# Performance work log

Measured on AMD Instinct MI355X. Metric: run time of the kernel, lower is better.

## Reference

```python
import jax, jax.numpy as jnp
import numpy as np

EPS = 1e-5  # BatchNorm2d default eps


def _binarize_ste(x):
    """Forward: sign(x). Backward: hardtanh STE (grad 1 where |x|<=1, else 0)."""
    xc = jnp.clip(x, -1.0, 1.0)
    return xc + jax.lax.stop_gradient(jnp.sign(x) - xc)


def setup_inputs() -> dict:
    key = jax.random.key(0)
    k1, k2, k3, k4 = jax.random.split(key, 4)
    x = jax.random.normal(k1, (32, 256, 32, 32), dtype=jnp.float32)
    # BatchNorm affine params (affine=True)
    gamma = 1.0 + 0.1 * jax.random.normal(k2, (256,), dtype=jnp.float32)
    beta = 0.1 * jax.random.normal(k3, (256,), dtype=jnp.float32)
    # Conv weight, OIHW, bias=False
    W = 0.05 * jax.random.normal(k4, (256, 256, 3, 3), dtype=jnp.float32)
    return {"x": x, "gamma": gamma, "beta": beta, "W": W}


def reference(x, gamma, beta, W):
    # BatchNorm2d, training-mode batch statistics over (N, H, W) per channel
    mean = jnp.mean(x, axis=(0, 2, 3), keepdims=True)
    var = jnp.var(x, axis=(0, 2, 3), keepdims=True)
    xn = (x - mean) * jax.lax.rsqrt(var + EPS)
    xn = xn * gamma[None, :, None, None] + beta[None, :, None, None]
    # Conv2d_1w1a: binarize activations and weights (sign fwd / STE bwd), then conv
    a = _binarize_ste(xn)
    wb = _binarize_ste(W)
    out = jax.lax.conv_general_dilated(
        a, wb,
        window_strides=(1, 1),
        padding=((1, 1), (1, 1)),
        dimension_numbers=("NCHW", "OIHW", "NCHW"),
    )
    return out
```

## Files before the change

### kernel.cpp

```cpp
#include <hip/hip_runtime.h>
#include <hip/hip_bf16.h>


#define NIMG 32
#define C    256
#define K    256

typedef int v4i  __attribute__((ext_vector_type(4)));
typedef int v16i __attribute__((ext_vector_type(16)));

#define AHT_IMG 295936
#define AHT_KB  36992
#define AHT_ROW 1088


__global__ __launch_bounds__(256) void k_stats_packw(
    const float* __restrict__ x, const float* __restrict__ W,
    double2* __restrict__ partials, char* __restrict__ wfrag) {
  int bx = blockIdx.x;
  int tid = threadIdx.x;
  if (bx >= 2048) {
    int k = bx - 2048, c = tid;
    const float* src = W + ((size_t)k * 256 + c) * 9;
    char* dst = wfrag + (size_t)(c >> 4) * 4096 + k * 16 + (c & 15);
    #pragma unroll
    for (int t = 0; t < 9; ++t)
      dst[(size_t)t * 65536] = (src[t] > 0.0f) ? (char)1 : (char)-1;
    return;
  }
  int c = bx >> 3, grp = bx & 7;
  double s = 0.0, sq = 0.0;
  #pragma unroll
  for (int ni = 0; ni < 4; ++ni) {
    int n = grp * 4 + ni;
    const float* p = x + (size_t)n * (C * 1024) + (size_t)c * 1024;
    float4 v = ((const float4*)p)[tid];
    s += (double)v.x + (double)v.y + (double)v.z + (double)v.w;
    sq += (double)v.x * v.x + (double)v.y * v.y
        + (double)v.z * v.z + (double)v.w * v.w;
  }
  for (int o = 32; o > 0; o >>= 1) {
    s += __shfl_down(s, o);
    sq += __shfl_down(sq, o);
  }
  __shared__ double ls[4], lq[4];
  if ((tid & 63) == 0) { ls[tid >> 6] = s; lq[tid >> 6] = sq; }
  __syncthreads();
  if (tid == 0) {
    double2 r;
    r.x = ls[0] + ls[1] + ls[2] + ls[3];
    r.y = lq[0] + lq[1] + lq[2] + lq[3];
    partials[c * 8 + grp] = r;
  }
}

__global__ __launch_bounds__(256) void k_packa_i8(
    const float* __restrict__ x, const double2* __restrict__ partials,
    const float* __restrict__ gamma, const float* __restrict__ beta,
    char* __restrict__ aHT) {
  __shared__ float lf[32 * 257];
  __shared__ float lthr[256];
  __shared__ unsigned lfl[256];
  int y = blockIdx.x, n = blockIdx.y, tid = threadIdx.x;

  {
    double S = 0.0, Q = 0.0;
    #pragma unroll
    for (int g = 0; g < 8; ++g) {
      double2 p = partials[tid * 8 + g];
      S += p.x; Q += p.y;
    }
    const double N = 32768.0;
    double mean = S / N;
    double var = Q / N - mean * mean;
    double rs = 1.0 / sqrt(var + 1e-5);
    double gm = (double)gamma[tid];
    double bt = (double)beta[tid];
    float t;
    unsigned flip;
    if (gm == 0.0) {
      t = (bt > 0.0) ? -3.0e38f : 3.0e38f;
      flip = 0u;
    } else {
      t = (float)(mean - bt / (rs * gm));
      flip = (gm < 0.0) ? 1u : 0u;
    }
    lthr[tid] = t;
    lfl[tid] = flip;
  }

  #pragma unroll
  for (int it = 0; it < 8; ++it) {
    int c = it * 32 + (tid >> 3), q = tid & 7;
    float4 v = *(const float4*)(x + (size_t)n * 262144 + (size_t)c * 1024
                                + y * 32 + q * 4);
    lf[(q * 4 + 0) * 257 + c] = v.x;
    lf[(q * 4 + 1) * 257 + c] = v.y;
    lf[(q * 4 + 2) * 257 + c] = v.z;
    lf[(q * 4 + 3) * 257 + c] = v.w;
  }
  __syncthreads();
  int xl = tid & 31, cb = tid >> 5;
  unsigned wds[8];
  #pragma unroll
  for (int g = 0; g < 8; ++g) {
    unsigned wv = 0;
    #pragma unroll
    for (int jj = 0; jj < 4; ++jj) {
      int c = cb * 32 + g * 4 + jj;
      float v = lf[xl * 257 + c];
      unsigned bit = ((v > lthr[c]) ? 1u : 0u) ^ lfl[c];
      unsigned byte = bit ? 0x01u : 0xFFu;
      wv |= byte << (8 * jj);
    }
    wds[g] = wv;
  }
  char* dst = aHT + ((size_t)n * 8 + cb) * AHT_KB
            + (size_t)(y + 1) * AHT_ROW + (size_t)(xl + 1) * 32;
  uint4 u0, u1;
  u0.x = wds[0]; u0.y = wds[1]; u0.z = wds[2]; u0.w = wds[3];
  u1.x = wds[4]; u1.y = wds[5]; u1.z = wds[6]; u1.w = wds[7];
  *(uint4*)dst = u0;
  *((uint4*)dst + 1) = u1;

  uint4 z; z.x = 0; z.y = 0; z.z = 0; z.w = 0;
  if (xl < 2) {
    char* hz = aHT + ((size_t)n * 8 + cb) * AHT_KB
             + (size_t)(y + 1) * AHT_ROW + (size_t)(xl * 33) * 32;
    *(uint4*)hz = z;
    *((uint4*)hz + 1) = z;
  }
  if (y == 0 || y == 31) {
    int row = (y == 0) ? 0 : 33;
    for (int idx = tid; idx < 272; idx += 256) {
      int kb = idx / 34, xx = idx % 34;
      char* hz = aHT + ((size_t)n * 8 + kb) * AHT_KB
               + (size_t)row * AHT_ROW + (size_t)xx * 32;
      *(uint4*)hz = z;
      *((uint4*)hz + 1) = z;
    }
  }
}

__global__ __launch_bounds__(512) void k_conv_mfma(
    const char* __restrict__ aHT, const char* __restrict__ wfrag,
    float* __restrict__ out) {
  int tid = threadIdx.x;
  int lane = tid & 63, w = tid >> 6;
  int nh = w & 3, mb = w >> 2;
  int bx = blockIdx.x;
  int lb = (bx & 7) * 32 + (bx >> 3);
  int n = lb >> 3, ys = lb & 7;
  int yw = ys * 4 + mb * 2;
  int xl = lane & 31, hi = lane >> 5;

  const char* abT = aHT + (size_t)n * AHT_IMG + (size_t)(xl + 1) * 32 + hi * 16;
  const char* wB = wfrag + hi * 4096 + (nh * 64 + xl) * 16;

  v16i a00 = {0}, a01 = {0}, a10 = {0}, a11 = {0};
  v4i cA00, cA01, cA10, cA11, nA00, nA01, nA10, nA11;
  v4i cB0, cB1, cB2, cB3, nB0, nB1, nB2, nB3;

  {
    const char* ab = abT + (size_t)yw * AHT_ROW - 32;
    cA00 = *(const v4i*)(ab);
    cA01 = *(const v4i*)(ab + AHT_ROW);
    cA10 = *(const v4i*)(ab + AHT_KB);
    cA11 = *(const v4i*)(ab + AHT_KB + AHT_ROW);
    cB0 = *(const v4i*)(wB);
    cB1 = *(const v4i*)(wB + 512);
    cB2 = *(const v4i*)(wB + 8192);
    cB3 = *(const v4i*)(wB + 8192 + 512);
  }

  for (int p = 0; p < 36; ++p) {
    if (p < 35) {
      int pp = p + 1;
      int tt = pp >> 2;
      int kb0 = (pp & 3) * 2;
      int dy = tt / 3 - 1, dx = tt % 3 - 1;
      const char* ab = abT + (size_t)kb0 * AHT_KB
                     + (size_t)(yw + dy + 1) * AHT_ROW + dx * 32;
      nA00 = *(const v4i*)(ab);
      nA01 = *(const v4i*)(ab + AHT_ROW);
      nA10 = *(const v4i*)(ab + AHT_KB);
      nA11 = *(const v4i*)(ab + AHT_KB + AHT_ROW);
      const char* wp2 = wB + (size_t)pp * 16384;
      nB0 = *(const v4i*)(wp2);
      nB1 = *(const v4i*)(wp2 + 512);
      nB2 = *(const v4i*)(wp2 + 8192);
      nB3 = *(const v4i*)(wp2 + 8192 + 512);
    }
    a00 = __builtin_amdgcn_mfma_i32_32x32x32_i8(cA00, cB0, a00, 0, 0, 0);
    a01 = __builtin_amdgcn_mfma_i32_32x32x32_i8(cA00, cB1, a01, 0, 0, 0);
    a10 = __builtin_amdgcn_mfma_i32_32x32x32_i8(cA01, cB0, a10, 0, 0, 0);
    a11 = __builtin_amdgcn_mfma_i32_32x32x32_i8(cA01, cB1, a11, 0, 0, 0);
    a00 = __builtin_amdgcn_mfma_i32_32x32x32_i8(cA10, cB2, a00, 0, 0, 0);
    a01 = __builtin_amdgcn_mfma_i32_32x32x32_i8(cA10, cB3, a01, 0, 0, 0);
    a10 = __builtin_amdgcn_mfma_i32_32x32x32_i8(cA11, cB2, a10, 0, 0, 0);
    a11 = __builtin_amdgcn_mfma_i32_32x32x32_i8(cA11, cB3, a11, 0, 0, 0);
    if (p < 35) {
      cA00 = nA00; cA01 = nA01; cA10 = nA10; cA11 = nA11;
      cB0 = nB0; cB1 = nB1; cB2 = nB2; cB3 = nB3;
    }
  }

  size_t ob0 = (size_t)n * 262144 + (size_t)(nh * 64 + xl) * 1024
             + (size_t)yw * 32 + 4 * hi;
  #pragma unroll
  for (int r = 0; r < 2; ++r) {
    #pragma unroll
    for (int nb = 0; nb < 2; ++nb) {
      v16i av = (r == 0) ? (nb == 0 ? a00 : a01) : (nb == 0 ? a10 : a11);
      float* obp = out + ob0 + (size_t)nb * 32768 + r * 32;
      #pragma unroll
      for (int q = 0; q < 4; ++q) {
        float4 f;
        f.x = (float)av[q * 4 + 0];
        f.y = (float)av[q * 4 + 1];
        f.z = (float)av[q * 4 + 2];
        f.w = (float)av[q * 4 + 3];
        *(float4*)(obp + 8 * q) = f;
      }
    }
  }
}


__global__ __launch_bounds__(256) void k_stats_part_fb(
    const float* __restrict__ x, double2* __restrict__ partials) {
  int grp = blockIdx.x;
  int c = blockIdx.y;
  int tid = threadIdx.x;
  double s = 0.0, sq = 0.0;
  #pragma unroll
  for (int ni = 0; ni < 4; ++ni) {
    int n = grp * 4 + ni;
    const float* p = x + (size_t)n * (C * 1024) + (size_t)c * 1024;
    float4 v = ((const float4*)p)[tid];
    s += (double)v.x + (double)v.y + (double)v.z + (double)v.w;
    sq += (double)v.x * v.x + (double)v.y * v.y
        + (double)v.z * v.z + (double)v.w * v.w;
  }
  for (int o = 32; o > 0; o >>= 1) {
    s += __shfl_down(s, o);
    sq += __shfl_down(sq, o);
  }
  __shared__ double ls[4], lq[4];
  if ((tid & 63) == 0) { ls[tid >> 6] = s; lq[tid >> 6] = sq; }
  __syncthreads();
  if (tid == 0) {
    double2 r;
    r.x = ls[0] + ls[1] + ls[2] + ls[3];
    r.y = lq[0] + lq[1] + lq[2] + lq[3];
    partials[c * 8 + grp] = r;
  }
}

__global__ __launch_bounds__(256) void k_packw_corr_final(
    const float* __restrict__ W, const double2* __restrict__ partials,
    const float* __restrict__ gamma, const float* __restrict__ beta,
    unsigned* __restrict__ wp, int* __restrict__ corr,
    unsigned* __restrict__ zp, float* __restrict__ t_out,
    unsigned* __restrict__ flip_out) {
  int bk = blockIdx.x;
  int tid = threadIdx.x;
  if (bk == 256) {
    int c = tid;
    double S = 0.0, Q = 0.0;
    #pragma unroll
    for (int g = 0; g < 8; ++g) {
      double2 p = partials[c * 8 + g];
      S += p.x; Q += p.y;
    }
    const double N = 32768.0;
    double mean = S / N;
    double var = Q / N - mean * mean;
    double rs = 1.0 / sqrt(var + 1e-5);
    double g = (double)gamma[c];
    double b = (double)beta[c];
    float t;
    unsigned flip;
    if (g == 0.0) {
      t = (b > 0.0) ? -3.0e38f : 3.0e38f;
      flip = 0u;
    } else {
      t = (float)(mean - b / (rs * g));
      flip = (g < 0.0) ? 1u : 0u;
    }
    t_out[c] = t;
    flip_out[c] = flip;
    return;
  }
  int k = bk;
  __shared__ unsigned lw[72];
  float w[9];
  const float* src = W + (size_t)k * 2304 + (size_t)tid * 9;
  #pragma unroll
  for (int t = 0; t < 9; ++t) w[t] = src[t];
  int lane = tid & 63, wv = tid >> 6;
  #pragma unroll
  for (int t = 0; t < 9; ++t) {
    unsigned long long m = __ballot(w[t] > 0.0f);
    if (lane == 0) {
      lw[t * 8 + 2 * wv] = (unsigned)m;
      lw[t * 8 + 2 * wv + 1] = (unsigned)(m >> 32);
    }
  }
  __syncthreads();
  if (tid < 72) wp[(size_t)k * 72 + tid] = lw[tid];
  if (tid >= 128 && tid < 144) {
    int cls = tid - 128;
    int sum = 0;
    #pragma unroll
    for (int t = 0; t < 9; ++t) {
      int dy = t / 3 - 1, dx = t % 3 - 1;
      bool inv = (((cls & 1) && dx == -1) || ((cls & 2) && dx == 1) ||
                  ((cls & 4) && dy == -1) || ((cls & 8) && dy == 1));
      if (inv) {
        #pragma unroll
        for (int j = 0; j < 8; ++j) sum += __popc(lw[t * 8 + j]);
      }
    }
    corr[k * 16 + cls] = sum;
  }
  if (bk == 0 && tid >= 192 && tid < 200) zp[tid - 192] = 0u;
}

__global__ __launch_bounds__(256) void k_packa_bits(
    const float* __restrict__ x, const float* __restrict__ t,
    const unsigned* __restrict__ flip, unsigned* __restrict__ ap) {
  int n = blockIdx.y;
  int p0 = blockIdx.x * 64;
  int pix = threadIdx.x & 63;
  int q = threadIdx.x >> 6;
  unsigned w0 = 0, w1 = 0;
  const float* xb = x + (size_t)n * (C * 1024) + p0 + pix;
  #pragma unroll
  for (int i = 0; i < 64; ++i) {
    int c = q * 64 + i;
    float tv = t[c];
    unsigned fl = flip[c];
    float v = xb[(size_t)c * 1024];
    unsigned bit = ((v > tv) ? 1u : 0u) ^ fl;
    if (i < 32) w0 |= bit << i;
    else        w1 |= bit << (i - 32);
  }
  uint2 st; st.x = w0; st.y = w1;
  *(uint2*)(ap + ((size_t)n * 1024 + p0 + pix) * 8 + q * 2) = st;
}

__global__ __launch_bounds__(256) void k_conv_pop(
    const unsigned* __restrict__ ap, const unsigned* __restrict__ wp,
    const int* __restrict__ corr, const unsigned* __restrict__ zp,
    float* __restrict__ out) {
  int n = blockIdx.z;
  int ystrip = blockIdx.y;
  int kc = blockIdx.x;
  int tid = threadIdx.x;
  int lane = tid & 63;
  int wave = tid >> 6;
  int y = ystrip * 8 + wave * 2 + (lane >> 5);
  int xx = lane & 31;
  int cls = (xx == 0 ? 1 : 0) | (xx == 31 ? 2 : 0) |
            (y == 0 ? 4 : 0) | (y == 31 ? 8 : 0);
  uint4 a0[9], a1[9];
  int nv = 0;
  const uint4* zp4 = (const uint4*)zp;
  #pragma unroll
  for (int t = 0; t < 9; ++t) {
    int dy = t / 3 - 1, dx = t % 3 - 1;
    int cy = y + dy, cx = xx + dx;
    bool valid = (cy >= 0) & (cy < 32) & (cx >= 0) & (cx < 32);
    nv += valid ? 1 : 0;
    const uint4* pa = valid
        ? (const uint4*)(ap + (((size_t)n * 32 + cy) * 32 + cx) * 8)
        : zp4;
    a0[t] = pa[0];
    a1[t] = pa[1];
  }
  int bias = nv << 8;
  float* ob = out + (size_t)n * (K * 1024) + (size_t)y * 32 + xx;
  for (int kk = 0; kk < 16; ++kk) {
    int k = kc * 16 + kk;
    const uint4* wq = (const uint4*)(wp + (size_t)k * 72);
    int s0 = 0, s1 = 0, s2 = 0, s3 = 0, s4 = 0, s5 = 0, s6 = 0, s7 = 0;
    #pragma unroll
    for (int t = 0; t < 9; ++t) {
      uint4 wa = wq[t * 2];
      uint4 wb = wq[t * 2 + 1];
      s0 += __popc(a0[t].x ^ wa.x);
      s1 += __popc(a0[t].y ^ wa.y);
      s2 += __popc(a0[t].z ^ wa.z);
      s3 += __popc(a0[t].w ^ wa.w);
      s4 += __popc(a1[t].x ^ wb.x);
      s5 += __popc(a1[t].y ^ wb.y);
      s6 += __popc(a1[t].z ^ wb.z);
      s7 += __popc(a1[t].w ^ wb.w);
    }
    int S = ((s0 + s1) + (s2 + s3)) + ((s4 + s5) + (s6 + s7));
    int tot = corr[(k << 4) + cls] - S;
    ob[(size_t)k * 1024] = (float)(bias + 2 * tot);
  }
}


extern "C" void kernel_launch(void* const* d_in, const int* in_sizes, int n_in,
                              void* d_out, int out_size, void* d_ws, size_t ws_size,
                              hipStream_t stream) {
  const float* x = (const float*)d_in[0];
  const float* gamma = (const float*)d_in[1];
  const float* beta = (const float*)d_in[2];
  const float* W = (const float*)d_in[3];
  float* out = (float*)d_out;
  char* ws = (char*)d_ws;

  const size_t NEED = 655360 + (size_t)NIMG * AHT_IMG;
  if (ws_size >= NEED) {
    double2* partials = (double2*)(ws + 4096);
    char* wfrag = ws + 36864;
    char* aHT = ws + 655360;

    k_stats_packw<<<2304, 256, 0, stream>>>(x, W, partials, wfrag);
    k_packa_i8<<<dim3(32, 32), 256, 0, stream>>>(x, partials, gamma, beta, aHT);
    k_conv_mfma<<<256, 512, 0, stream>>>(aHT, wfrag, out);
  } else {
    float* t = (float*)ws;
    unsigned* flip = (unsigned*)(ws + 1024);
    unsigned* wp = (unsigned*)(ws + 4096);
    unsigned* zp = (unsigned*)(ws + 77824);
    int* corr = (int*)(ws + 78336);
    double2* partials = (double2*)(ws + 98304);
    unsigned* ap = (unsigned*)(ws + 131072);

    k_stats_part_fb<<<dim3(8, 256), 256, 0, stream>>>(x, partials);
    k_packw_corr_final<<<257, 256, 0, stream>>>(W, partials, gamma, beta,
                                                wp, corr, zp, t, flip);
    k_packa_bits<<<dim3(16, 32), 256, 0, stream>>>(x, t, flip, ap);
    k_conv_pop<<<dim3(16, 4, 32), 256, 0, stream>>>(ap, wp, corr, zp, out);
  }
}
```

Baseline: 49.87 us.

## Stage conv A/B tiles in LDS via async global_load_lds double buffering

Rewrites the conv MFMA main loop so each step's activation and weight fragments are copied from global memory straight into a double-buffered LDS tile with global_load_lds. Warps then read their operands from LDS instead of issuing redundant per-warp global loads. Operands that several warps share are fetched once per block, cutting global/L2 traffic. The cost is 48KB of shared memory per block, which may limit occupancy, plus a block-wide barrier every iteration.

```diff
diff --git a/kernel.cpp b/kernel.cpp
--- a/kernel.cpp
+++ b/kernel.cpp
@@ -12,6 +12,10 @@
 #define AHT_IMG 295936
 #define AHT_KB  36992
 #define AHT_ROW 1088
+
+#define GL16(gp, lp) __builtin_amdgcn_global_load_lds(                        \
+    (const __attribute__((address_space(1))) unsigned int*)(gp),              \
+    (__attribute__((address_space(3))) unsigned int*)(lp), 16, 0, 0)
 
 
 __global__ __launch_bounds__(256) void k_stats_packw(
@@ -145,64 +149,74 @@
 __global__ __launch_bounds__(512) void k_conv_mfma(
     const char* __restrict__ aHT, const char* __restrict__ wfrag,
     float* __restrict__ out) {
+  __shared__ char As[49152];
   int tid = threadIdx.x;
   int lane = tid & 63, w = tid >> 6;
   int nh = w & 3, mb = w >> 2;
   int bx = blockIdx.x;
   int lb = (bx & 7) * 32 + (bx >> 3);
   int n = lb >> 3, ys = lb & 7;
-  int yw = ys * 4 + mb * 2;
+  int y0 = ys * 4;
+  int yw = y0 + mb * 2;
   int xl = lane & 31, hi = lane >> 5;
 
-  const char* abT = aHT + (size_t)n * AHT_IMG + (size_t)(xl + 1) * 32 + hi * 16;
-  const char* wB = wfrag + hi * 4096 + (nh * 64 + xl) * 16;
+  int sr = w >> 1, skb = w & 1;
+  int sp = lane & 31, sh = lane >> 5;
+  const char* aLane = aHT + (size_t)n * AHT_IMG + (size_t)skb * AHT_KB
+                    + (size_t)sp * 32 + sh * 16;
+
+  unsigned aRd = (unsigned)(mb * 4096 + hi * 512 + xl * 16);
+  unsigned bRd = (unsigned)(hi * 4096 + (nh * 64 + xl) * 16);
 
   v16i a00 = {0}, a01 = {0}, a10 = {0}, a11 = {0};
-  v4i cA00, cA01, cA10, cA11, nA00, nA01, nA10, nA11;
-  v4i cB0, cB1, cB2, cB3, nB0, nB1, nB2, nB3;
 
   {
-    const char* ab = abT + (size_t)yw * AHT_ROW - 32;
-    cA00 = *(const v4i*)(ab);
-    cA01 = *(const v4i*)(ab + AHT_ROW);
-    cA10 = *(const v4i*)(ab + AHT_KB);
-    cA11 = *(const v4i*)(ab + AHT_KB + AHT_ROW);
-    cB0 = *(const v4i*)(wB);
-    cB1 = *(const v4i*)(wB + 512);
-    cB2 = *(const v4i*)(wB + 8192);
-    cB3 = *(const v4i*)(wB + 8192 + 512);
-  }
+    const char* ag = aLane + (size_t)(y0 + 0 + sr) * AHT_ROW + 0;
+    GL16(ag, As + w * 1024);
+    const char* bg = wfrag + (size_t)(2 * w) * 1024 + lane * 16;
+    GL16(bg, As + 8192 + (2 * w) * 1024);
+    GL16(bg + 1024, As + 8192 + (2 * w + 1) * 1024);
+  }
+  __syncthreads();
 
   for (int p = 0; p < 36; ++p) {
+    int cur = (p & 1) * 24576;
     if (p < 35) {
+      int nxt = 24576 - cur;
       int pp = p + 1;
       int tt = pp >> 2;
       int kb0 = (pp & 3) * 2;
       int dy = tt / 3 - 1, dx = tt % 3 - 1;
-      const char* ab = abT + (size_t)kb0 * AHT_KB
-                     + (size_t)(yw + dy + 1) * AHT_ROW + dx * 32;
-      nA00 = *(const v4i*)(ab);
-      nA01 = *(const v4i*)(ab + AHT_ROW);
-      nA10 = *(const v4i*)(ab + AHT_KB);
-      nA11 = *(const v4i*)(ab + AHT_KB + AHT_ROW);
-      const char* wp2 = wB + (size_t)pp * 16384;
-      nB0 = *(const v4i*)(wp2);
-      nB1 = *(const v4i*)(wp2 + 512);
-      nB2 = *(const v4i*)(wp2 + 8192);
-      nB3 = *(const v4i*)(wp2 + 8192 + 512);
-    }
-    a00 = __builtin_amdgcn_mfma_i32_32x32x32_i8(cA00, cB0, a00, 0, 0, 0);
-    a01 = __builtin_amdgcn_mfma_i32_32x32x32_i8(cA00, cB1, a01, 0, 0, 0);
-    a10 = __builtin_amdgcn_mfma_i32_32x32x32_i8(cA01, cB0, a10, 0, 0, 0);
-    a11 = __builtin_amdgcn_mfma_i32_32x32x32_i8(cA01, cB1, a11, 0, 0, 0);
-    a00 = __builtin_amdgcn_mfma_i32_32x32x32_i8(cA10, cB2, a00, 0, 0, 0);
-    a01 = __builtin_amdgcn_mfma_i32_32x32x32_i8(cA10, cB3, a01, 0, 0, 0);
-    a10 = __builtin_amdgcn_mfma_i32_32x32x32_i8(cA11, cB2, a10, 0, 0, 0);
-    a11 = __builtin_amdgcn_mfma_i32_32x32x32_i8(cA11, cB3, a11, 0, 0, 0);
-    if (p < 35) {
-      cA00 = nA00; cA01 = nA01; cA10 = nA10; cA11 = nA11;
-      cB0 = nB0; cB1 = nB1; cB2 = nB2; cB3 = nB3;
-    }
+      const char* ag = aLane + (size_t)kb0 * AHT_KB
+                     + (size_t)(y0 + 1 + dy + sr) * AHT_ROW
+                     + (size_t)(1 + dx) * 32;
+      GL16(ag, As + nxt + w * 1024);
+      const char* bg = wfrag + (size_t)pp * 16384 + (size_t)(2 * w) * 1024
+                     + lane * 16;
+      GL16(bg, As + nxt + 8192 + (2 * w) * 1024);
+      GL16(bg + 1024, As + nxt + 8192 + (2 * w + 1) * 1024);
+    }
+    {
+      const char* cb = As + cur;
+      v4i A00 = *(const v4i*)(cb + aRd);
+      v4i A01 = *(const v4i*)(cb + aRd + 1024);
+      v4i A10 = *(const v4i*)(cb + aRd + 2048);
+      v4i A11 = *(const v4i*)(cb + aRd + 3072);
+      const char* bb = cb + 8192;
+      v4i B0 = *(const v4i*)(bb + bRd);
+      v4i B1 = *(const v4i*)(bb + bRd + 512);
+      v4i B2 = *(const v4i*)(bb + bRd + 8192);
+      v4i B3 = *(const v4i*)(bb + bRd + 8192 + 512);
+      a00 = __builtin_amdgcn_mfma_i32_32x32x32_i8(A00, B0, a00, 0, 0, 0);
+      a01 = __builtin_amdgcn_mfma_i32_32x32x32_i8(A00, B1, a01, 0, 0, 0);
+      a10 = __builtin_amdgcn_mfma_i32_32x32x32_i8(A10, B0, a10, 0, 0, 0);
+      a11 = __builtin_amdgcn_mfma_i32_32x32x32_i8(A10, B1, a11, 0, 0, 0);
+      a00 = __builtin_amdgcn_mfma_i32_32x32x32_i8(A01, B2, a00, 0, 0, 0);
+      a01 = __builtin_amdgcn_mfma_i32_32x32x32_i8(A01, B3, a01, 0, 0, 0);
+      a10 = __builtin_amdgcn_mfma_i32_32x32x32_i8(A11, B2, a10, 0, 0, 0);
+      a11 = __builtin_amdgcn_mfma_i32_32x32x32_i8(A11, B3, a11, 0, 0, 0);
+    }
+    __syncthreads();
   }
 
   size_t ob0 = (size_t)n * 262144 + (size_t)(nh * 64 + xl) * 1024
```

Result: slower. 53.98 us (+8.2%).

## Stage activation halo tile in LDS and deepen weight prefetch

Applied to the files above, without the earlier changes.

The conv kernel now cooperatively copies the block's binarized activation tile (6 rows with halo, all 8 channel blocks, 34 columns) into about 52KB of shared memory once. It then reads the A fragments for each tap from LDS instead of issuing repeated global loads per tap. Weight fragments are now prefetched two iterations ahead instead of one. This trades roughly 9x redundant global/L2 traffic for LDS reads plus a barrier, but the large LDS footprint may reduce occupancy and the LDS access pattern may cause bank conflicts.

```diff
diff --git a/kernel.cpp b/kernel.cpp
--- a/kernel.cpp
+++ b/kernel.cpp
@@ -145,65 +145,73 @@
 __global__ __launch_bounds__(512) void k_conv_mfma(
     const char* __restrict__ aHT, const char* __restrict__ wfrag,
     float* __restrict__ out) {
+  __shared__ uint4 As4[3264];
+  char* As = (char*)As4;
   int tid = threadIdx.x;
   int lane = tid & 63, w = tid >> 6;
   int nh = w & 3, mb = w >> 2;
   int bx = blockIdx.x;
   int lb = (bx & 7) * 32 + (bx >> 3);
   int n = lb >> 3, ys = lb & 7;
-  int yw = ys * 4 + mb * 2;
+  int y0 = ys * 4;
+  int yw = y0 + mb * 2;
   int xl = lane & 31, hi = lane >> 5;
 
-  const char* abT = aHT + (size_t)n * AHT_IMG + (size_t)(xl + 1) * 32 + hi * 16;
+  {
+    const char* aImg = aHT + (size_t)n * AHT_IMG;
+    for (int e = tid; e < 3264; e += 512) {
+      int px = e % 34;
+      int q = e / 34;
+      int hs = q & 1;
+      int q2 = q >> 1;
+      int rl = q2 % 6;
+      int kb = q2 / 6;
+      const char* g = aImg + (size_t)kb * AHT_KB
+                    + (size_t)(y0 + rl) * AHT_ROW + px * 32 + hs * 16;
+      *(v4i*)(As + (size_t)e * 16) = *(const v4i*)g;
+    }
+  }
+  __syncthreads();
+
   const char* wB = wfrag + hi * 4096 + (nh * 64 + xl) * 16;
+  int aBase = (mb * 2 + 1) * 1088 + hi * 544 + (xl + 1) * 16;
 
   v16i a00 = {0}, a01 = {0}, a10 = {0}, a11 = {0};
-  v4i cA00, cA01, cA10, cA11, nA00, nA01, nA10, nA11;
-  v4i cB0, cB1, cB2, cB3, nB0, nB1, nB2, nB3;
-
-  {
-    const char* ab = abT + (size_t)yw * AHT_ROW - 32;
-    cA00 = *(const v4i*)(ab);
-    cA01 = *(const v4i*)(ab + AHT_ROW);
-    cA10 = *(const v4i*)(ab + AHT_KB);
-    cA11 = *(const v4i*)(ab + AHT_KB + AHT_ROW);
-    cB0 = *(const v4i*)(wB);
-    cB1 = *(const v4i*)(wB + 512);
-    cB2 = *(const v4i*)(wB + 8192);
-    cB3 = *(const v4i*)(wB + 8192 + 512);
-  }
+  v4i c0, c1, c2, c3, d0, d1, d2, d3, e0, e1, e2, e3;
+
+  #define LOADB(P, R0, R1, R2, R3)                                            \
+    { const char* bp_ = wB + (size_t)(P) * 16384;                             \
+      R0 = *(const v4i*)(bp_);                                                \
+      R1 = *(const v4i*)(bp_ + 512);                                          \
+      R2 = *(const v4i*)(bp_ + 8192);                                         \
+      R3 = *(const v4i*)(bp_ + 8704); }
+
+  LOADB(0, c0, c1, c2, c3);
+  LOADB(1, d0, d1, d2, d3);
 
   for (int p = 0; p < 36; ++p) {
+    if (p < 34) LOADB(p + 2, e0, e1, e2, e3);
+    int tap = p >> 2, kb0 = (p & 3) * 2;
+    int dy = tap / 3 - 1, dx = tap % 3 - 1;
+    int ab = aBase + kb0 * 6528 + dy * 1088 + dx * 16;
+    v4i Ar0k0 = *(const v4i*)(As + ab);
+    v4i Ar1k0 = *(const v4i*)(As + ab + 1088);
+    v4i Ar0k1 = *(const v4i*)(As + ab + 6528);
+    v4i Ar1k1 = *(const v4i*)(As + ab + 6528 + 1088);
+    a00 = __builtin_amdgcn_mfma_i32_32x32x32_i8(Ar0k0, c0, a00, 0, 0, 0);
+    a01 = __builtin_amdgcn_mfma_i32_32x32x32_i8(Ar0k0, c1, a01, 0, 0, 0);
+    a10 = __builtin_amdgcn_mfma_i32_32x32x32_i8(Ar1k0, c0, a10, 0, 0, 0);
+    a11 = __builtin_amdgcn_mfma_i32_32x32x32_i8(Ar1k0, c1, a11, 0, 0, 0);
+    a00 = __builtin_amdgcn_mfma_i32_32x32x32_i8(Ar0k1, c2, a00, 0, 0, 0);
+    a01 = __builtin_amdgcn_mfma_i32_32x32x32_i8(Ar0k1, c3, a01, 0, 0, 0);
+    a10 = __builtin_amdgcn_mfma_i32_32x32x32_i8(Ar1k1, c2, a10, 0, 0, 0);
+    a11 = __builtin_amdgcn_mfma_i32_32x32x32_i8(Ar1k1, c3, a11, 0, 0, 0);
     if (p < 35) {
-      int pp = p + 1;
-      int tt = pp >> 2;
-      int kb0 = (pp & 3) * 2;
-      int dy = tt / 3 - 1, dx = tt % 3 - 1;
-      const char* ab = abT + (size_t)kb0 * AHT_KB
-                     + (size_t)(yw + dy + 1) * AHT_ROW + dx * 32;
-      nA00 = *(const v4i*)(ab);
-      nA01 = *(const v4i*)(ab + AHT_ROW);
-      nA10 = *(const v4i*)(ab + AHT_KB);
-      nA11 = *(const v4i*)(ab + AHT_KB + AHT_ROW);
-      const char* wp2 = wB + (size_t)pp * 16384;
-      nB0 = *(const v4i*)(wp2);
-      nB1 = *(const v4i*)(wp2 + 512);
-      nB2 = *(const v4i*)(wp2 + 8192);
-      nB3 = *(const v4i*)(wp2 + 8192 + 512);
-    }
-    a00 = __builtin_amdgcn_mfma_i32_32x32x32_i8(cA00, cB0, a00, 0, 0, 0);
-    a01 = __builtin_amdgcn_mfma_i32_32x32x32_i8(cA00, cB1, a01, 0, 0, 0);
-    a10 = __builtin_amdgcn_mfma_i32_32x32x32_i8(cA01, cB0, a10, 0, 0, 0);
-    a11 = __builtin_amdgcn_mfma_i32_32x32x32_i8(cA01, cB1, a11, 0, 0, 0);
-    a00 = __builtin_amdgcn_mfma_i32_32x32x32_i8(cA10, cB2, a00, 0, 0, 0);
-    a01 = __builtin_amdgcn_mfma_i32_32x32x32_i8(cA10, cB3, a01, 0, 0, 0);
-    a10 = __builtin_amdgcn_mfma_i32_32x32x32_i8(cA11, cB2, a10, 0, 0, 0);
-    a11 = __builtin_amdgcn_mfma_i32_32x32x32_i8(cA11, cB3, a11, 0, 0, 0);
-    if (p < 35) {
-      cA00 = nA00; cA01 = nA01; cA10 = nA10; cA11 = nA11;
-      cB0 = nB0; cB1 = nB1; cB2 = nB2; cB3 = nB3;
-    }
-  }
+      c0 = d0; c1 = d1; c2 = d2; c3 = d3;
+      d0 = e0; d1 = e1; d2 = e2; d3 = e3;
+    }
+  }
+  #undef LOADB
 
   size_t ob0 = (size_t)n * 262144 + (size_t)(nh * 64 + xl) * 1024
              + (size_t)yw * 32 + 4 * hi;
```

New measurement: 49.19 us. About the same (-1.4%).
